# Optimization experiments

Hardware: AMD Instinct MI355X
Metric: run time of the kernel (lower is better)

## Reference

```python
import jax, jax.numpy as jnp
import numpy as np

INPUT_SIZE = 1024
HIDDEN_SIZE = 2048
BATCH = 4096


def _xavier(key, shape):
    fan_out, fan_in = shape
    std = jnp.sqrt(2.0 / (fan_in + fan_out)).astype(jnp.float32)
    return jax.random.normal(key, shape, dtype=jnp.float32) * std


def setup_inputs() -> dict:
    key = jax.random.key(0)
    ks = jax.random.split(key, 8)
    return {
        "x": jax.random.normal(ks[0], (BATCH, INPUT_SIZE), dtype=jnp.float32),
        "hprev": jax.random.normal(ks[1], (BATCH, HIDDEN_SIZE), dtype=jnp.float32),
        "Wh": _xavier(ks[2], (HIDDEN_SIZE, INPUT_SIZE)),
        "Wz": _xavier(ks[3], (HIDDEN_SIZE, INPUT_SIZE)),
        "Wr": _xavier(ks[4], (HIDDEN_SIZE, INPUT_SIZE)),
        "Uh": _xavier(ks[5], (HIDDEN_SIZE, HIDDEN_SIZE)),
        "Uz": _xavier(ks[6], (HIDDEN_SIZE, HIDDEN_SIZE)),
        "Ur": _xavier(ks[7], (HIDDEN_SIZE, HIDDEN_SIZE)),
        "bh": jnp.zeros((HIDDEN_SIZE,), dtype=jnp.float32),
        "bz": jnp.zeros((HIDDEN_SIZE,), dtype=jnp.float32),
        "br": jnp.zeros((HIDDEN_SIZE,), dtype=jnp.float32),
    }


def reference(x, hprev, Wh, Wz, Wr, Uh, Uz, Ur, bh, bz, br):
    # batched matvec: (b,i) @ (h,i)^T -> (b,h)
    r = jax.nn.sigmoid(x @ Wr.T + hprev @ Ur.T + br)
    z = jax.nn.sigmoid(x @ Wz.T + hprev @ Uz.T + bz)
    h_proposed = jnp.tanh(x @ Wh.T + (r * hprev) @ Uh.T + bh)
    return z * h_proposed + (1.0 - z) * hprev
```

## Files before the change

kernel.cpp:

```cpp
#include <hip/hip_runtime.h>

#define BATCH 4096
#define ISZ   1024
#define HSZ   2048

typedef __bf16 bf16x8 __attribute__((ext_vector_type(8)));
typedef float  f32x4  __attribute__((ext_vector_type(4)));

__device__ __forceinline__ unsigned short f2bf(float f) {
  unsigned u = __builtin_bit_cast(unsigned, f);
  u += 0x7fffu + ((u >> 16) & 1u);
  return (unsigned short)(u >> 16);
}

struct CvtArgs {
  const float* src[8];
  unsigned short* dst[8];
  int cum[9];
};

__global__ __launch_bounds__(256) void cvt_all_kernel(CvtArgs a, int total4) {
  int i = blockIdx.x * 256 + threadIdx.x;
  if (i >= total4) return;
  int s = 0;
#pragma unroll
  for (int k = 0; k < 7; ++k) s += (i >= a.cum[k + 1]) ? 1 : 0;
  int off = i - a.cum[s];
  float4 f = ((const float4*)a.src[s])[off];
  ushort4 o;
  o.x = f2bf(f.x); o.y = f2bf(f.y); o.z = f2bf(f.z); o.w = f2bf(f.w);
  ((ushort4*)a.dst[s])[off] = o;
}

__device__ __forceinline__ void stage_tile64(const unsigned short* __restrict__ g, int ldK,
                                             int tileRow, int k0, char* lds, int t) {
  char* l0 = lds + ((t >> 6) << 10);
#pragma unroll
  for (int k = 0; k < 4; ++k) {
    int linear = t + k * 256;
    int row = linear >> 3;
    int cs  = linear & 7;
    int c   = cs ^ (row & 7);
    const unsigned short* gp = g + (size_t)(tileRow + row) * ldK + (k0 + c * 8);
    __builtin_amdgcn_global_load_lds((const __attribute__((address_space(1))) void*)gp,
                                     (__attribute__((address_space(3))) void*)(l0 + k * 4096),
                                     16, 0, 0);
  }
}

__device__ __forceinline__ void gemm_seg(const unsigned short* __restrict__ A,
                                         const unsigned short* __restrict__ W,
                                         int K, int rowBase, int colBase,
                                         char* ldsA, char* ldsB,
                                         f32x4 (&acc)[4][4], int t) {
  const int lane = t & 63;
  const int wid  = t >> 6;
  const int wm   = wid >> 1, wn = wid & 1;
  const int lrow = lane & 15;
  const int quad = lane >> 4;
  const int r7   = lrow & 7;
  for (int k0 = 0; k0 < K; k0 += 64) {
    stage_tile64(A, K, rowBase, k0, ldsA, t);
    stage_tile64(W, K, colBase, k0, ldsB, t);
    __syncthreads();
#pragma unroll
    for (int kk = 0; kk < 2; ++kk) {
      const int swz = (((kk << 2) | quad) ^ r7) * 16;
      bf16x8 af[4], bfr[4];
#pragma unroll
      for (int i = 0; i < 4; ++i) {
        int ra = wm * 64 + i * 16 + lrow;
        int rb = wn * 64 + i * 16 + lrow;
        af[i]  = *(const bf16x8*)(ldsA + ra * 128 + swz);
        bfr[i] = *(const bf16x8*)(ldsB + rb * 128 + swz);
      }
#pragma unroll
      for (int i = 0; i < 4; ++i)
#pragma unroll
        for (int j = 0; j < 4; ++j)
          acc[i][j] = __builtin_amdgcn_mfma_f32_16x16x32_bf16(af[i], bfr[j], acc[i][j], 0, 0, 0);
    }
    __syncthreads();
  }
}

__device__ __forceinline__ float fast_sigmoid(float v) {
  return 1.0f / (1.0f + __expf(-v));
}
__device__ __forceinline__ float fast_tanh(float v) {
  float e = __expf(2.0f * v);
  return 1.0f - 2.0f / (e + 1.0f);
}

__global__ __launch_bounds__(256) void gate_rz(
    const unsigned short* __restrict__ xb, const unsigned short* __restrict__ hb,
    const unsigned short* __restrict__ Wr, const unsigned short* __restrict__ Ur,
    const unsigned short* __restrict__ Wz, const unsigned short* __restrict__ Uz,
    const float* __restrict__ br, const float* __restrict__ bz,
    const float* __restrict__ hprev,
    unsigned short* __restrict__ rh, float* __restrict__ Zbuf) {
  __shared__ char lds[32768];
  char* ldsA = lds;
  char* ldsB = lds + 16384;
  const int t = threadIdx.x;
  const int rowBase = blockIdx.y * 128;
  const int colBase = blockIdx.x * 128;
  const bool isZ = (blockIdx.z != 0);
  const unsigned short* W = isZ ? Wz : Wr;
  const unsigned short* U = isZ ? Uz : Ur;
  const float* bias = isZ ? bz : br;

  f32x4 acc[4][4];
#pragma unroll
  for (int i = 0; i < 4; ++i)
#pragma unroll
    for (int j = 0; j < 4; ++j)
      acc[i][j] = (f32x4){0.f, 0.f, 0.f, 0.f};

  gemm_seg(xb, W, ISZ, rowBase, colBase, ldsA, ldsB, acc, t);
  gemm_seg(hb, U, HSZ, rowBase, colBase, ldsA, ldsB, acc, t);

  const int lane = t & 63, wid = t >> 6;
  const int wm = wid >> 1, wn = wid & 1, lrow = lane & 15, quad = lane >> 4;
#pragma unroll
  for (int i = 0; i < 4; ++i) {
#pragma unroll
    for (int j = 0; j < 4; ++j) {
      int col = colBase + wn * 64 + j * 16 + lrow;
      float bv = bias[col];
#pragma unroll
      for (int r = 0; r < 4; ++r) {
        int row = rowBase + wm * 64 + i * 16 + quad * 4 + r;
        float s = fast_sigmoid(acc[i][j][r] + bv);
        int idx = row * HSZ + col;
        if (isZ) {
          Zbuf[idx] = s;
        } else {
          rh[idx] = f2bf(s * hprev[idx]);
        }
      }
    }
  }
}

__global__ __launch_bounds__(256) void gate_h(
    const unsigned short* __restrict__ xb, const unsigned short* __restrict__ rhb,
    const unsigned short* __restrict__ Wh, const unsigned short* __restrict__ Uh,
    const float* __restrict__ bh, const float* __restrict__ Zbuf,
    const float* __restrict__ hprev, float* __restrict__ out) {
  __shared__ char lds[32768];
  char* ldsA = lds;
  char* ldsB = lds + 16384;
  const int t = threadIdx.x;
  const int rowBase = blockIdx.y * 128;
  const int colBase = blockIdx.x * 128;

  f32x4 acc[4][4];
#pragma unroll
  for (int i = 0; i < 4; ++i)
#pragma unroll
    for (int j = 0; j < 4; ++j)
      acc[i][j] = (f32x4){0.f, 0.f, 0.f, 0.f};

  gemm_seg(xb, Wh, ISZ, rowBase, colBase, ldsA, ldsB, acc, t);
  gemm_seg(rhb, Uh, HSZ, rowBase, colBase, ldsA, ldsB, acc, t);

  const int lane = t & 63, wid = t >> 6;
  const int wm = wid >> 1, wn = wid & 1, lrow = lane & 15, quad = lane >> 4;
#pragma unroll
  for (int i = 0; i < 4; ++i) {
#pragma unroll
    for (int j = 0; j < 4; ++j) {
      int col = colBase + wn * 64 + j * 16 + lrow;
      float bv = bh[col];
#pragma unroll
      for (int r = 0; r < 4; ++r) {
        int row = rowBase + wm * 64 + i * 16 + quad * 4 + r;
        float hp = fast_tanh(acc[i][j][r] + bv);
        int idx = row * HSZ + col;
        float z = Zbuf[idx];
        float h = hprev[idx];
        out[idx] = h + z * (hp - h);
      }
    }
  }
}

extern "C" void kernel_launch(void* const* d_in, const int* in_sizes, int n_in,
                              void* d_out, int out_size, void* d_ws, size_t ws_size,
                              hipStream_t stream) {
  (void)in_sizes; (void)n_in; (void)out_size; (void)ws_size;
  const float* x     = (const float*)d_in[0];
  const float* hprev = (const float*)d_in[1];
  const float* Wh    = (const float*)d_in[2];
  const float* Wz    = (const float*)d_in[3];
  const float* Wr    = (const float*)d_in[4];
  const float* Uh    = (const float*)d_in[5];
  const float* Uz    = (const float*)d_in[6];
  const float* Ur    = (const float*)d_in[7];
  const float* bh    = (const float*)d_in[8];
  const float* bz    = (const float*)d_in[9];
  const float* br    = (const float*)d_in[10];
  float* out = (float*)d_out;

  char* ws = (char*)d_ws;
  size_t off = 0;
  auto alloc = [&](size_t bytes) { char* p = ws + off; off += bytes; return p; };
  unsigned short* xb  = (unsigned short*)alloc((size_t)BATCH * ISZ * 2);
  unsigned short* hb  = (unsigned short*)alloc((size_t)BATCH * HSZ * 2);
  unsigned short* Wrb = (unsigned short*)alloc((size_t)HSZ * ISZ * 2);
  unsigned short* Wzb = (unsigned short*)alloc((size_t)HSZ * ISZ * 2);
  unsigned short* Whb = (unsigned short*)alloc((size_t)HSZ * ISZ * 2);
  unsigned short* Urb = (unsigned short*)alloc((size_t)HSZ * HSZ * 2);
  unsigned short* Uzb = (unsigned short*)alloc((size_t)HSZ * HSZ * 2);
  unsigned short* Uhb = (unsigned short*)alloc((size_t)HSZ * HSZ * 2);
  unsigned short* rhb = (unsigned short*)alloc((size_t)BATCH * HSZ * 2);
  float*          Zb  = (float*)alloc((size_t)BATCH * HSZ * 4);

  CvtArgs ca;
  const float* srcs[8]      = {x, hprev, Wr, Wz, Wh, Ur, Uz, Uh};
  unsigned short* dsts[8]   = {xb, hb, Wrb, Wzb, Whb, Urb, Uzb, Uhb};
  int n4s[8] = {BATCH * ISZ / 4, BATCH * HSZ / 4,
                HSZ * ISZ / 4, HSZ * ISZ / 4, HSZ * ISZ / 4,
                HSZ * HSZ / 4, HSZ * HSZ / 4, HSZ * HSZ / 4};
  int cum = 0;
  for (int i = 0; i < 8; ++i) {
    ca.src[i] = srcs[i];
    ca.dst[i] = dsts[i];
    ca.cum[i] = cum;
    cum += n4s[i];
  }
  ca.cum[8] = cum;
  cvt_all_kernel<<<(cum + 255) / 256, 256, 0, stream>>>(ca, cum);

  dim3 gridA(HSZ / 128, BATCH / 128, 2);
  gate_rz<<<gridA, 256, 0, stream>>>(xb, hb, Wrb, Urb, Wzb, Uzb, br, bz, hprev, rhb, Zb);

  dim3 gridB(HSZ / 128, BATCH / 128, 1);
  gate_h<<<gridB, 256, 0, stream>>>(xb, rhb, Whb, Uhb, bh, Zb, hprev, out);
}
```

Before: 379.7 us.

## Store Z in bf16, reuse bf16 hprev for r*h, remap blocks per XCD

The Z gate buffer is now stored as bf16 instead of fp32, and r*hprev reads the already-converted bf16 hprev instead of the fp32 input. This halves the intermediate traffic in the epilogues. Block indices are remapped so that consecutive blocks dispatched to the same XCD share column tiles, which should improve L2 reuse of the weights. Launch bounds now request 4 blocks per CU. The cost is extra bf16 rounding of z and of hprev in the gate product.

After: 347.3 us. 1.09x faster.

```diff
diff --git a/kernel.cpp b/kernel.cpp
--- a/kernel.cpp
+++ b/kernel.cpp
@@ -11,6 +11,10 @@
   unsigned u = __builtin_bit_cast(unsigned, f);
   u += 0x7fffu + ((u >> 16) & 1u);
   return (unsigned short)(u >> 16);
+}
+__device__ __forceinline__ float bf2f(unsigned short s) {
+  unsigned u = ((unsigned)s) << 16;
+  return __builtin_bit_cast(float, u);
 }
 
 struct CvtArgs {
@@ -92,23 +96,29 @@
   return 1.0f - 2.0f / (e + 1.0f);
 }
 
-__global__ __launch_bounds__(256) void gate_rz(
+__global__ __launch_bounds__(256, 4) void gate_rz(
     const unsigned short* __restrict__ xb, const unsigned short* __restrict__ hb,
     const unsigned short* __restrict__ Wr, const unsigned short* __restrict__ Ur,
     const unsigned short* __restrict__ Wz, const unsigned short* __restrict__ Uz,
     const float* __restrict__ br, const float* __restrict__ bz,
-    const float* __restrict__ hprev,
-    unsigned short* __restrict__ rh, float* __restrict__ Zbuf) {
+    unsigned short* __restrict__ rh, unsigned short* __restrict__ Zbuf) {
   __shared__ char lds[32768];
   char* ldsA = lds;
   char* ldsB = lds + 16384;
   const int t = threadIdx.x;
-  const int rowBase = blockIdx.y * 128;
-  const int colBase = blockIdx.x * 128;
-  const bool isZ = (blockIdx.z != 0);
+
+  int lin = blockIdx.x + (blockIdx.y << 4) + (blockIdx.z << 9);
+  int xcd = lin & 7, s = lin >> 3;
+  int bx = xcd * 2 + (s & 1);
+  int by = (s >> 1) & 31;
+  int bz_ = s >> 6;
+
+  const int rowBase = by * 128;
+  const int colBase = bx * 128;
+  const bool isZ = (bz_ != 0);
   const unsigned short* W = isZ ? Wz : Wr;
   const unsigned short* U = isZ ? Uz : Ur;
-  const float* bias = isZ ? bz : br;
+  const float* biasP = isZ ? bz : br;
 
   f32x4 acc[4][4];
 #pragma unroll
@@ -127,33 +137,39 @@
 #pragma unroll
     for (int j = 0; j < 4; ++j) {
       int col = colBase + wn * 64 + j * 16 + lrow;
-      float bv = bias[col];
+      float bv = biasP[col];
 #pragma unroll
       for (int r = 0; r < 4; ++r) {
         int row = rowBase + wm * 64 + i * 16 + quad * 4 + r;
-        float s = fast_sigmoid(acc[i][j][r] + bv);
+        float sg = fast_sigmoid(acc[i][j][r] + bv);
         int idx = row * HSZ + col;
         if (isZ) {
-          Zbuf[idx] = s;
+          Zbuf[idx] = f2bf(sg);
         } else {
-          rh[idx] = f2bf(s * hprev[idx]);
+          rh[idx] = f2bf(sg * bf2f(hb[idx]));
         }
       }
     }
   }
 }
 
-__global__ __launch_bounds__(256) void gate_h(
+__global__ __launch_bounds__(256, 4) void gate_h(
     const unsigned short* __restrict__ xb, const unsigned short* __restrict__ rhb,
     const unsigned short* __restrict__ Wh, const unsigned short* __restrict__ Uh,
-    const float* __restrict__ bh, const float* __restrict__ Zbuf,
+    const float* __restrict__ bh, const unsigned short* __restrict__ Zbuf,
     const float* __restrict__ hprev, float* __restrict__ out) {
   __shared__ char lds[32768];
   char* ldsA = lds;
   char* ldsB = lds + 16384;
   const int t = threadIdx.x;
-  const int rowBase = blockIdx.y * 128;
-  const int colBase = blockIdx.x * 128;
+
+  int lin = blockIdx.x + (blockIdx.y << 4);
+  int xcd = lin & 7, s = lin >> 3;
+  int bx = xcd * 2 + (s & 1);
+  int by = s >> 1;
+
+  const int rowBase = by * 128;
+  const int colBase = bx * 128;
 
   f32x4 acc[4][4];
 #pragma unroll
@@ -178,7 +194,7 @@
         int row = rowBase + wm * 64 + i * 16 + quad * 4 + r;
         float hp = fast_tanh(acc[i][j][r] + bv);
         int idx = row * HSZ + col;
-        float z = Zbuf[idx];
+        float z = bf2f(Zbuf[idx]);
         float h = hprev[idx];
         out[idx] = h + z * (hp - h);
       }
@@ -215,7 +231,7 @@
   unsigned short* Uzb = (unsigned short*)alloc((size_t)HSZ * HSZ * 2);
   unsigned short* Uhb = (unsigned short*)alloc((size_t)HSZ * HSZ * 2);
   unsigned short* rhb = (unsigned short*)alloc((size_t)BATCH * HSZ * 2);
-  float*          Zb  = (float*)alloc((size_t)BATCH * HSZ * 4);
+  unsigned short* Zb  = (unsigned short*)alloc((size_t)BATCH * HSZ * 2);
 
   CvtArgs ca;
   const float* srcs[8]      = {x, hprev, Wr, Wz, Wh, Ur, Uz, Uh};
@@ -234,7 +250,7 @@
   cvt_all_kernel<<<(cum + 255) / 256, 256, 0, stream>>>(ca, cum);
 
   dim3 gridA(HSZ / 128, BATCH / 128, 2);
-  gate_rz<<<gridA, 256, 0, stream>>>(xb, hb, Wrb, Urb, Wzb, Uzb, br, bz, hprev, rhb, Zb);
+  gate_rz<<<gridA, 256, 0, stream>>>(xb, hb, Wrb, Urb, Wzb, Uzb, br, bz, rhb, Zb);
 
   dim3 gridB(HSZ / 128, BATCH / 128, 1);
   gate_h<<<gridB, 256, 0, stream>>>(xb, rhb, Whb, Uhb, bh, Zb, hprev, out);
```
